# Kernel tuning notes

Measured on AMD Instinct MI355X. Metric: run time of the kernel, lower is better.

Reference implementation:

```python
import jax, jax.numpy as jnp
import numpy as np

B, CIN, COUT, H, W = 64, 64, 64, 32, 32
K, STRIDE, PAD = 3, 1, 1
HOUT = (H + 2 * PAD - K) // STRIDE + 1
WOUT = (W + 2 * PAD - K) // STRIDE + 1


def setup_inputs() -> dict:
    key = jax.random.key(0)
    k1, k2, k3 = jax.random.split(key, 3)
    x = jax.random.normal(k1, (B, CIN, H, W), dtype=jnp.float32)
    # weight: per-location filters (leading singleton batch dim of the torch
    # param is dropped; it only served broadcasting)
    weight = jax.random.normal(k2, (CIN, COUT, HOUT, WOUT, K, K), dtype=jnp.float32)
    bias = jax.random.normal(k3, (COUT, HOUT, WOUT), dtype=jnp.float32)
    return {"x": x, "weight": weight, "bias": bias}


def _extract_patches(x, k, stride, pad, hout, wout):
    # x: [B, C, H, W] -> patches [B, C, k*k, hout, wout]
    xp = jnp.pad(x, ((0, 0), (0, 0), (pad, pad), (pad, pad)))
    slabs = [
        xp[:, :, i : i + (hout - 1) * stride + 1 : stride,
               j : j + (wout - 1) * stride + 1 : stride]
        for i in range(k) for j in range(k)
    ]
    return jnp.stack(slabs, axis=2)


def reference(x, weight, bias):
    cin, cout, hout, wout, k, _ = weight.shape
    patches = _extract_patches(x, k, STRIDE, PAD, hout, wout)  # [B, Cin, k*k, Ho, Wo]
    w = weight.reshape(cin, cout, hout, wout, k * k)
    # fused per-location dot product: avoids the [B,Cin,Cout,Ho,Wo,k,k] intermediate
    y = jnp.einsum('bikhw,iohwk->bohw', patches, w) + bias[None]
    return y
```

## Files before the change

kernel.cpp:

```cpp
#include <hip/hip_runtime.h>
#include <hip/hip_bf16.h>


#define B_    64
#define HW_   32
#define HP_   34
#define NLOC  1024
#define W_OST 9216u
#define W_IST 589824u
#define XT_BYTES  ((size_t)64*HP_*HP_*64*2)
#define WS_NEED   (XT_BYTES)

typedef __attribute__((ext_vector_type(8))) short short8;
typedef __attribute__((ext_vector_type(8))) unsigned short ushort8;
typedef __attribute__((ext_vector_type(4))) float floatx4;

static __device__ __forceinline__ unsigned short f2bf(float f) {
  __hip_bfloat16 h = __float2bfloat16(f);
  return __builtin_bit_cast(unsigned short, h);
}

static __device__ __forceinline__ void soft_barrier() {
  __asm__ volatile("s_waitcnt lgkmcnt(0)" ::: "memory");
  __builtin_amdgcn_s_barrier();
}

__global__ __launch_bounds__(256) void xpose_pad(const float* __restrict__ x,
                                                 unsigned short* __restrict__ xt) {
  int bid = blockIdx.x;
  int i = bid / HP_, hh = bid % HP_;
  __shared__ float tile[B_ * 33];
  int t = threadIdx.x;
  bool interior = (hh >= 1 && hh <= HW_);
  if (interior) {
    int h = hh - 1, w = t & 31, bs = t >> 5;
    #pragma unroll
    for (int r = 0; r < 8; ++r) {
      int b = r * 8 + bs;
      tile[b * 33 + w] = x[(((size_t)b * 64 + i) * HW_ + h) * HW_ + w];
    }
  }
  __syncthreads();
  int b = t & 63, wsb = t >> 6;
  size_t base = (size_t)(i * HP_ + hh) * HP_ * B_;
  #pragma unroll
  for (int s = 0; s < 9; ++s) {
    int ww = s * 4 + wsb;
    if (ww < HP_) {
      float v = 0.f;
      if (interior && ww >= 1 && ww <= HW_) v = tile[b * 33 + (ww - 1)];
      xt[base + (size_t)ww * B_ + b] = f2bf(v);
    }
  }
}

__global__ __launch_bounds__(256, 2) void lc2d_fused(
    const unsigned short* __restrict__ xt,
    const float* __restrict__ wsrc,
    const float* __restrict__ bias,
    float* __restrict__ out) {
  __shared__ __align__(16) unsigned short Af[2][16 * 64 * 8];
  __shared__ __align__(16) unsigned short Bf[2][8 * 64 * 8];
  __shared__ __align__(16) unsigned short Bs[16 * 64 * 8];
  __shared__ __align__(16) unsigned short scr[4][2][512];

  const int bid   = blockIdx.x;
  const int lt    = ((bid & 7) << 6) | (bid >> 3);
  const int ohalf = lt & 1;
  const int loc0  = (lt >> 1) << 2;
  const int tid   = threadIdx.x;
  const int lane  = tid & 63;
  const int ll    = tid >> 6;
  const int loc   = loc0 + ll;
  const int hblk  = loc >> 5, wblk = loc & 31;
  const int col   = lane & 15;
  const int quad  = lane >> 4;
  const int o_0   = ohalf * 32 + col;

  floatx4 acc[4][2];
  {
    float b0 = bias[(unsigned)o_0 * 1024u + (unsigned)loc];
    float b1 = bias[(unsigned)(o_0 + 16) * 1024u + (unsigned)loc];
    #pragma unroll
    for (int mt = 0; mt < 4; ++mt) {
      acc[mt][0] = (floatx4){b0, b0, b0, b0};
      acc[mt][1] = (floatx4){b1, b1, b1, b1};
    }
  }

  floatx4 wa[5], wb[5];
  const bool lastok = (tid < 128);
  const size_t wrow = (size_t)loc0 * 9;
  const unsigned obase = (unsigned)ohalf * 32u;

  auto issueW = [&](int c, floatx4 (&wreg)[5]) {
    const int i0 = c << 2;
    #pragma unroll
    for (int r = 0; r < 5; ++r) {
      if (r < 4 || lastok) {
        int idx = r * 256 + tid;
        int g = idx / 9, p = idx - g * 9;
        int i = i0 + (g >> 5), o = (int)obase + (g & 31);
        wreg[r] = *(const floatx4*)(wsrc + (size_t)i * W_IST + (size_t)o * W_OST
                                    + wrow + (size_t)(p * 4));
      }
    }
  };
  auto scatterW = [&](int c, floatx4 (&wreg)[5], unsigned short* bfp) {
    const int i0 = c << 2;
    #pragma unroll
    for (int r = 0; r < 5; ++r) {
      if (r < 4 || lastok) {
        int idx = r * 256 + tid;
        int g = idx / 9, p = idx - g * 9;
        int iq = g >> 5, ol = g & 31;
        int ot = ol >> 4, oc = ol & 15;
        int flane = iq * 16 + oc;
        #pragma unroll
        for (int e = 0; e < 4; ++e) {
          int fi = p * 4 + e;
          int lle = fi / 9, kk = fi - lle * 9;
          unsigned short v = f2bf(wreg[r][e]);
          if (kk < 8) {
            bfp[((lle * 2 + ot) * 64 + flane) * 8 + kk] = v;
          } else {
            int i = i0 + iq;
            int sc = i >> 5, k2 = i & 31;
            Bs[(((lle * 2 + sc) * 2 + ot) * 64 + (k2 >> 3) * 16 + oc) * 8 + (k2 & 7)] = v;
          }
        }
      }
    }
  };

  auto xtLoad = [&](int t, int q) -> ushort8 {
    int i, kh, kw;
    if (t < 16) {
      i = (t << 2) + q;
      int kk = lane >> 3;
      kh = kk / 3; kw = kk - kh * 3;
    } else {
      i = ((t - 16) << 5) + (q << 3) + (lane >> 3);
      kh = 2; kw = 2;
    }
    return *(const ushort8*)(xt +
        (((unsigned)i * HP_ + (unsigned)(hblk + kh)) * HP_ + (unsigned)(wblk + kw)) * 64u
        + ((unsigned)(lane & 7) << 3));
  };
  auto xposePair = [&](ushort8 v0, ushort8 v1, int q0, unsigned short* afp) {
    *(ushort8*)&scr[ll][0][lane << 3] = v0;
    *(ushort8*)&scr[ll][1][lane << 3] = v1;
    __asm__ volatile("s_waitcnt lgkmcnt(0)" ::: "memory");
    ushort8 p0, p1;
    #pragma unroll
    for (int jr = 0; jr < 8; ++jr) p0[jr] = scr[ll][0][jr * 64 + lane];
    #pragma unroll
    for (int jr = 0; jr < 8; ++jr) p1[jr] = scr[ll][1][jr * 64 + lane];
    __asm__ volatile("s_waitcnt lgkmcnt(0)" ::: "memory");
    *(ushort8*)(afp + (size_t)((((ll << 2) + (lane >> 4)) << 6)
                               + (q0 << 4) + (lane & 15)) * 8) = p0;
    *(ushort8*)(afp + (size_t)((((ll << 2) + (lane >> 4)) << 6)
                               + ((q0 + 1) << 4) + (lane & 15)) * 8) = p1;
  };

  auto doMFMA = [&](const unsigned short* afp, const unsigned short* bbase, int boff) {
    ushort8 a0 = *(const ushort8*)(afp + (size_t)(((ll << 2) + 0) * 64 + lane) * 8);
    ushort8 a1 = *(const ushort8*)(afp + (size_t)(((ll << 2) + 1) * 64 + lane) * 8);
    ushort8 a2 = *(const ushort8*)(afp + (size_t)(((ll << 2) + 2) * 64 + lane) * 8);
    ushort8 a3 = *(const ushort8*)(afp + (size_t)(((ll << 2) + 3) * 64 + lane) * 8);
    ushort8 b0 = *(const ushort8*)(bbase + (size_t)((boff + 0) * 64 + lane) * 8);
    ushort8 b1 = *(const ushort8*)(bbase + (size_t)((boff + 1) * 64 + lane) * 8);
    acc[0][0] = __builtin_amdgcn_mfma_f32_16x16x32_bf16(
        __builtin_bit_cast(short8, a0), __builtin_bit_cast(short8, b0), acc[0][0], 0, 0, 0);
    acc[1][0] = __builtin_amdgcn_mfma_f32_16x16x32_bf16(
        __builtin_bit_cast(short8, a1), __builtin_bit_cast(short8, b0), acc[1][0], 0, 0, 0);
    acc[2][0] = __builtin_amdgcn_mfma_f32_16x16x32_bf16(
        __builtin_bit_cast(short8, a2), __builtin_bit_cast(short8, b0), acc[2][0], 0, 0, 0);
    acc[3][0] = __builtin_amdgcn_mfma_f32_16x16x32_bf16(
        __builtin_bit_cast(short8, a3), __builtin_bit_cast(short8, b0), acc[3][0], 0, 0, 0);
    acc[0][1] = __builtin_amdgcn_mfma_f32_16x16x32_bf16(
        __builtin_bit_cast(short8, a0), __builtin_bit_cast(short8, b1), acc[0][1], 0, 0, 0);
    acc[1][1] = __builtin_amdgcn_mfma_f32_16x16x32_bf16(
        __builtin_bit_cast(short8, a1), __builtin_bit_cast(short8, b1), acc[1][1], 0, 0, 0);
    acc[2][1] = __builtin_amdgcn_mfma_f32_16x16x32_bf16(
        __builtin_bit_cast(short8, a2), __builtin_bit_cast(short8, b1), acc[2][1], 0, 0, 0);
    acc[3][1] = __builtin_amdgcn_mfma_f32_16x16x32_bf16(
        __builtin_bit_cast(short8, a3), __builtin_bit_cast(short8, b1), acc[3][1], 0, 0, 0);
  };

  issueW(0, wa);
  {
    ushort8 v0 = xtLoad(0, 0), v1 = xtLoad(0, 1);
    ushort8 v2 = xtLoad(0, 2), v3 = xtLoad(0, 3);
    xposePair(v0, v1, 0, &Af[0][0]);
    xposePair(v2, v3, 2, &Af[0][0]);
  }
  scatterW(0, wa, &Bf[0][0]);
  issueW(1, wb);
  soft_barrier();

#define STEP(C, WI, WS) do {                                                  \
    const int c_ = (C);                                                       \
    ushort8 xv0 = xtLoad(c_ + 1, 0), xv1 = xtLoad(c_ + 1, 1);                 \
    ushort8 xv2 = xtLoad(c_ + 1, 2), xv3 = xtLoad(c_ + 1, 3);                 \
    if (c_ + 2 <= 15) issueW(c_ + 2, WI);                                     \
    doMFMA(&Af[c_ & 1][0], &Bf[c_ & 1][0], ll << 1);                          \
    xposePair(xv0, xv1, 0, &Af[(c_ & 1) ^ 1][0]);                             \
    xposePair(xv2, xv3, 2, &Af[(c_ & 1) ^ 1][0]);                             \
    if (c_ + 1 <= 15) scatterW(c_ + 1, WS, &Bf[(c_ & 1) ^ 1][0]);             \
    soft_barrier();                                                           \
  } while (0)

  #pragma unroll 1
  for (int cc = 0; cc < 16; cc += 2) {
    STEP(cc,     wa, wb);
    STEP(cc + 1, wb, wa);
  }
#undef STEP

  {
    ushort8 xv0 = xtLoad(17, 0), xv1 = xtLoad(17, 1);
    ushort8 xv2 = xtLoad(17, 2), xv3 = xtLoad(17, 3);
    doMFMA(&Af[0][0], &Bs[0], (ll << 1) << 1);
    xposePair(xv0, xv1, 0, &Af[1][0]);
    xposePair(xv2, xv3, 2, &Af[1][0]);
    soft_barrier();
    doMFMA(&Af[1][0], &Bs[0], ((ll << 1) + 1) << 1);
  }

  #pragma unroll
  for (int mt = 0; mt < 4; ++mt) {
    int b = mt * 16 + quad * 4;
    #pragma unroll
    for (int r = 0; r < 4; ++r) {
      out[((unsigned)(b + r) * 64u + (unsigned)o_0) * 1024u + (unsigned)loc] = acc[mt][0][r];
      out[((unsigned)(b + r) * 64u + (unsigned)(o_0 + 16)) * 1024u + (unsigned)loc] = acc[mt][1][r];
    }
  }
}

__global__ __launch_bounds__(256, 4) void lc2d_fallback(
    const float* __restrict__ x, const float* __restrict__ weight,
    const float* __restrict__ bias, float* __restrict__ out) {
  int t0 = blockIdx.x;
  int loc = ((t0 & 7) << 7) | (t0 >> 3);
  int h = loc >> 5, w = loc & 31;
  int tid = threadIdx.x;
  int b = tid & 63;
  int o0 = (tid >> 6) * 16;
  __shared__ float As[72 * 64];
  float acc[16];
  #pragma unroll
  for (int j = 0; j < 16; ++j) acc[j] = bias[(size_t)(o0 + j) * NLOC + loc];
  for (int ic = 0; ic < 8; ++ic) {
    __syncthreads();
    #pragma unroll
    for (int s = 0; s < 18; ++s) {
      int f = s * 256 + tid;
      int k = f >> 6, lb = f & 63;
      int kk = k >> 3, isub = k & 7;
      int i = ic * 8 + isub;
      int kh = kk / 3, kw = kk - kh * 3;
      int hh = h + kh - 1, ww = w + kw - 1;
      float v = (hh >= 0 && hh < HW_ && ww >= 0 && ww < HW_)
                  ? x[(((size_t)lb * 64 + i) * HW_ + hh) * HW_ + ww] : 0.f;
      As[k * 64 + lb] = v;
    }
    __syncthreads();
    #pragma unroll 1
    for (int isub = 0; isub < 8; ++isub) {
      const float* wp = weight + (size_t)(ic * 8 + isub) * W_IST
                               + (size_t)o0 * W_OST + loc * 9;
      #pragma unroll
      for (int kk = 0; kk < 9; ++kk) {
        float a = As[(kk * 8 + isub) * 64 + b];
        #pragma unroll
        for (int j = 0; j < 16; ++j)
          acc[j] = fmaf(a, wp[(size_t)j * W_OST + kk], acc[j]);
      }
    }
  }
  size_t ob = ((size_t)b * 64 + o0) * NLOC + loc;
  #pragma unroll
  for (int j = 0; j < 16; ++j) out[ob + (size_t)j * NLOC] = acc[j];
}

extern "C" void kernel_launch(void* const* d_in, const int* in_sizes, int n_in,
                              void* d_out, int out_size, void* d_ws, size_t ws_size,
                              hipStream_t stream) {
  const float* x  = (const float*)d_in[0];
  const float* wt = (const float*)d_in[1];
  const float* bs = (const float*)d_in[2];
  float* out = (float*)d_out;

  if (ws_size >= WS_NEED) {
    unsigned short* xtb = (unsigned short*)d_ws;
    xpose_pad<<<64 * HP_, 256, 0, stream>>>(x, xtb);
    lc2d_fused<<<512, 256, 0, stream>>>(xtb, wt, bs, out);
  } else {
    lc2d_fallback<<<NLOC, 256, 0, stream>>>(x, wt, bs, out);
  }
}
```

Baseline: 252.2 us.

## Single-buffer A tile in per-wave LDS to raise occupancy to three blocks

Result: slower. 384.1 us (+52.3%).

```diff
diff --git a/kernel.cpp b/kernel.cpp
--- a/kernel.cpp
+++ b/kernel.cpp
@@ -54,15 +54,15 @@
   }
 }
 
-__global__ __launch_bounds__(256, 2) void lc2d_fused(
+__global__ __launch_bounds__(256, 3) void lc2d_fused(
     const unsigned short* __restrict__ xt,
     const float* __restrict__ wsrc,
     const float* __restrict__ bias,
     float* __restrict__ out) {
-  __shared__ __align__(16) unsigned short Af[2][16 * 64 * 8];
+  __shared__ __align__(16) unsigned short Af[16 * 64 * 8];
   __shared__ __align__(16) unsigned short Bf[2][8 * 64 * 8];
   __shared__ __align__(16) unsigned short Bs[16 * 64 * 8];
-  __shared__ __align__(16) unsigned short scr[4][2][512];
+  __shared__ __align__(16) unsigned short scr[4][512];
 
   const int bid   = blockIdx.x;
   const int lt    = ((bid & 7) << 6) | (bid >> 3);
@@ -147,27 +147,22 @@
         (((unsigned)i * HP_ + (unsigned)(hblk + kh)) * HP_ + (unsigned)(wblk + kw)) * 64u
         + ((unsigned)(lane & 7) << 3));
   };
-  auto xposePair = [&](ushort8 v0, ushort8 v1, int q0, unsigned short* afp) {
-    *(ushort8*)&scr[ll][0][lane << 3] = v0;
-    *(ushort8*)&scr[ll][1][lane << 3] = v1;
-    __asm__ volatile("s_waitcnt lgkmcnt(0)" ::: "memory");
-    ushort8 p0, p1;
-    #pragma unroll
-    for (int jr = 0; jr < 8; ++jr) p0[jr] = scr[ll][0][jr * 64 + lane];
-    #pragma unroll
-    for (int jr = 0; jr < 8; ++jr) p1[jr] = scr[ll][1][jr * 64 + lane];
-    __asm__ volatile("s_waitcnt lgkmcnt(0)" ::: "memory");
-    *(ushort8*)(afp + (size_t)((((ll << 2) + (lane >> 4)) << 6)
-                               + (q0 << 4) + (lane & 15)) * 8) = p0;
-    *(ushort8*)(afp + (size_t)((((ll << 2) + (lane >> 4)) << 6)
-                               + ((q0 + 1) << 4) + (lane & 15)) * 8) = p1;
-  };
-
-  auto doMFMA = [&](const unsigned short* afp, const unsigned short* bbase, int boff) {
-    ushort8 a0 = *(const ushort8*)(afp + (size_t)(((ll << 2) + 0) * 64 + lane) * 8);
-    ushort8 a1 = *(const ushort8*)(afp + (size_t)(((ll << 2) + 1) * 64 + lane) * 8);
-    ushort8 a2 = *(const ushort8*)(afp + (size_t)(((ll << 2) + 2) * 64 + lane) * 8);
-    ushort8 a3 = *(const ushort8*)(afp + (size_t)(((ll << 2) + 3) * 64 + lane) * 8);
+  auto xposeRole = [&](ushort8 v, int q) {
+    *(ushort8*)&scr[ll][lane << 3] = v;
+    __asm__ volatile("s_waitcnt lgkmcnt(0)" ::: "memory");
+    ushort8 p;
+    #pragma unroll
+    for (int jr = 0; jr < 8; ++jr) p[jr] = scr[ll][jr * 64 + lane];
+    __asm__ volatile("s_waitcnt lgkmcnt(0)" ::: "memory");
+    *(ushort8*)(&Af[0] + (size_t)((((ll << 2) + (lane >> 4)) << 6)
+                                  + (q << 4) + (lane & 15)) * 8) = p;
+  };
+
+  auto doMFMA = [&](const unsigned short* bbase, int boff) {
+    ushort8 a0 = *(const ushort8*)(&Af[0] + (size_t)(((ll << 2) + 0) * 64 + lane) * 8);
+    ushort8 a1 = *(const ushort8*)(&Af[0] + (size_t)(((ll << 2) + 1) * 64 + lane) * 8);
+    ushort8 a2 = *(const ushort8*)(&Af[0] + (size_t)(((ll << 2) + 2) * 64 + lane) * 8);
+    ushort8 a3 = *(const ushort8*)(&Af[0] + (size_t)(((ll << 2) + 3) * 64 + lane) * 8);
     ushort8 b0 = *(const ushort8*)(bbase + (size_t)((boff + 0) * 64 + lane) * 8);
     ushort8 b1 = *(const ushort8*)(bbase + (size_t)((boff + 1) * 64 + lane) * 8);
     acc[0][0] = __builtin_amdgcn_mfma_f32_16x16x32_bf16(
@@ -189,26 +184,24 @@
   };
 
   issueW(0, wa);
-  {
-    ushort8 v0 = xtLoad(0, 0), v1 = xtLoad(0, 1);
-    ushort8 v2 = xtLoad(0, 2), v3 = xtLoad(0, 3);
-    xposePair(v0, v1, 0, &Af[0][0]);
-    xposePair(v2, v3, 2, &Af[0][0]);
-  }
+  ushort8 xv0 = xtLoad(0, 0), xv1 = xtLoad(0, 1);
+  ushort8 xv2 = xtLoad(0, 2), xv3 = xtLoad(0, 3);
   scatterW(0, wa, &Bf[0][0]);
   issueW(1, wb);
   soft_barrier();
 
 #define STEP(C, WI, WS) do {                                                  \
     const int c_ = (C);                                                       \
-    ushort8 xv0 = xtLoad(c_ + 1, 0), xv1 = xtLoad(c_ + 1, 1);                 \
-    ushort8 xv2 = xtLoad(c_ + 1, 2), xv3 = xtLoad(c_ + 1, 3);                 \
+    ushort8 nx0 = xtLoad(c_ + 1, 0), nx1 = xtLoad(c_ + 1, 1);                 \
+    ushort8 nx2 = xtLoad(c_ + 1, 2), nx3 = xtLoad(c_ + 1, 3);                 \
     if (c_ + 2 <= 15) issueW(c_ + 2, WI);                                     \
-    doMFMA(&Af[c_ & 1][0], &Bf[c_ & 1][0], ll << 1);                          \
-    xposePair(xv0, xv1, 0, &Af[(c_ & 1) ^ 1][0]);                             \
-    xposePair(xv2, xv3, 2, &Af[(c_ & 1) ^ 1][0]);                             \
+    xposeRole(xv0, 0); xposeRole(xv1, 1);                                     \
+    xposeRole(xv2, 2); xposeRole(xv3, 3);                                     \
+    __asm__ volatile("s_waitcnt lgkmcnt(0)" ::: "memory");                    \
+    doMFMA(&Bf[c_ & 1][0], ll << 1);                                          \
     if (c_ + 1 <= 15) scatterW(c_ + 1, WS, &Bf[(c_ & 1) ^ 1][0]);             \
     soft_barrier();                                                           \
+    xv0 = nx0; xv1 = nx1; xv2 = nx2; xv3 = nx3;                               \
   } while (0)
 
   #pragma unroll 1
@@ -219,13 +212,17 @@
 #undef STEP
 
   {
-    ushort8 xv0 = xtLoad(17, 0), xv1 = xtLoad(17, 1);
-    ushort8 xv2 = xtLoad(17, 2), xv3 = xtLoad(17, 3);
-    doMFMA(&Af[0][0], &Bs[0], (ll << 1) << 1);
-    xposePair(xv0, xv1, 0, &Af[1][0]);
-    xposePair(xv2, xv3, 2, &Af[1][0]);
-    soft_barrier();
-    doMFMA(&Af[1][0], &Bs[0], ((ll << 1) + 1) << 1);
+    ushort8 nx0 = xtLoad(17, 0), nx1 = xtLoad(17, 1);
+    ushort8 nx2 = xtLoad(17, 2), nx3 = xtLoad(17, 3);
+    xposeRole(xv0, 0); xposeRole(xv1, 1);
+    xposeRole(xv2, 2); xposeRole(xv3, 3);
+    __asm__ volatile("s_waitcnt lgkmcnt(0)" ::: "memory");
+    doMFMA(&Bs[0], (ll << 1) << 1);
+    __asm__ volatile("s_waitcnt lgkmcnt(0)" ::: "memory");
+    xposeRole(nx0, 0); xposeRole(nx1, 1);
+    xposeRole(nx2, 2); xposeRole(nx3, 3);
+    __asm__ volatile("s_waitcnt lgkmcnt(0)" ::: "memory");
+    doMFMA(&Bs[0], ((ll << 1) + 1) << 1);
   }
 
   #pragma unroll
```
